# Performance work log

Hardware: AMD Instinct MI355X
Metric: run time of the kernel (lower is better)

Reference implementation:

```python
import jax, jax.numpy as jnp
import numpy as np

N_NODES = 100000
N_EDGES = 1600000
IN_F, HID, EMB = 128, 64, 32


def setup_inputs() -> dict:
    key = jax.random.key(0)
    ks = jax.random.split(key, 10)
    x = jax.random.normal(ks[0], (N_NODES, IN_F), dtype=jnp.float32)
    edge_index = jax.random.randint(ks[1], (2, N_EDGES), 0, N_NODES, dtype=jnp.int64)
    s = lambda k, sh, fan_in: jax.random.normal(k, sh, dtype=jnp.float32) / jnp.sqrt(jnp.float32(fan_in))
    return {
        "x": x,
        "edge_index": edge_index,
        # SAGEConv1: lin_l (applied to aggregated neighbors, with bias) + lin_r (root, no bias)
        "W1_l": s(ks[2], (IN_F, HID), IN_F), "b1": jnp.zeros((HID,), jnp.float32), "W1_r": s(ks[3], (IN_F, HID), IN_F),
        # SAGEConv2
        "W2_l": s(ks[4], (HID, EMB), HID), "b2": jnp.zeros((EMB,), jnp.float32), "W2_r": s(ks[5], (HID, EMB), HID),
        # risk head
        "Wh": s(ks[6], (EMB, 1), EMB), "bh": jnp.zeros((1,), jnp.float32),
    }


def _sage_conv(x, src, dst, W_l, b, W_r):
    # gather messages from source nodes, segment-mean at destination nodes
    msg_sum = jax.ops.segment_sum(x[src], dst, num_segments=N_NODES)  # [N, F]
    cnt = jax.ops.segment_sum(jnp.ones((src.shape[0],), x.dtype), dst, num_segments=N_NODES)
    mean_agg = msg_sum / jnp.maximum(cnt, 1.0)[:, None]  # isolated nodes -> 0
    return mean_agg @ W_l + b + x @ W_r


def reference(x, edge_index, W1_l, b1, W1_r, W2_l, b2, W2_r, Wh, bh):
    src, dst = edge_index[0], edge_index[1]
    h = jax.nn.relu(_sage_conv(x, src, dst, W1_l, b1, W1_r))
    # dropout is identity in eval mode
    embeddings = jax.nn.relu(_sage_conv(h, src, dst, W2_l, b2, W2_r))
    risk_scores = embeddings @ Wh + bh
    return embeddings, risk_scores
```

## Files before the change

kernel.cpp:

```cpp
#include <hip/hip_runtime.h>
#include <hip/hip_bf16.h>

#define N_NODES 100000
#define N_EDGES 1600000
#define NBUCK   196
#define BSHIFT  9
#define BCAP    12288

typedef __bf16 bf16x8 __attribute__((ext_vector_type(8)));
typedef float  f32x4  __attribute__((ext_vector_type(4)));
typedef float  f32x2  __attribute__((ext_vector_type(2)));


__device__ inline unsigned char enc_fp8(float v) {
    return (unsigned char)(__builtin_amdgcn_cvt_pk_fp8_f32(v, v, 0, 0) & 0xFF);
}

__global__ __launch_bounds__(256) void partition_k(const int* __restrict__ ei,
                                                   int* __restrict__ gcur,
                                                   unsigned* __restrict__ bbuf) {
    __shared__ int hist[NBUCK];
    __shared__ int cur[NBUCK];
    int t = threadIdx.x;
    for (int i = t; i < NBUCK; i += 256) hist[i] = 0;
    __syncthreads();
    int base = blockIdx.x * 4096;
    unsigned pk[16];
    int bk[16];
#pragma unroll
    for (int i = 0; i < 16; ++i) {
        int e = base + t + i * 256;
        if (e < N_EDGES) {
            int s = ei[e], d = ei[N_EDGES + e];
            int b = d >> BSHIFT;
            pk[i] = ((unsigned)(d & 511) << 17) | (unsigned)s;
            bk[i] = b;
            atomicAdd(&hist[b], 1);
        } else bk[i] = -1;
    }
    __syncthreads();
    for (int i = t; i < NBUCK; i += 256)
        cur[i] = atomicAdd(&gcur[i], hist[i]);
    __syncthreads();
#pragma unroll
    for (int i = 0; i < 16; ++i) {
        if (bk[i] >= 0) {
            int pos = atomicAdd(&cur[bk[i]], 1);
            bbuf[(size_t)bk[i] * BCAP + pos] = pk[i];
        }
    }
}

__global__ __launch_bounds__(256) void csr_gemm1_k(const unsigned* __restrict__ bbuf,
                                                   const int* __restrict__ gcur,
                                                   int* __restrict__ cnt,
                                                   int* __restrict__ offsets,
                                                   int* __restrict__ csr,
                                                   const float* __restrict__ x,
                                                   const float* __restrict__ W1l,
                                                   const float* __restrict__ W1r,
                                                   unsigned char* __restrict__ c1l,
                                                   __bf16* __restrict__ c1r) {
    __shared__ __align__(16) char smem[34816];
    int t = threadIdx.x;
    if (blockIdx.x < NBUCK) {
        int* lcnt = (int*)smem;
        int* loff = (int*)(smem + 2048);
        int* lcur = (int*)(smem + 4096);
        int* ssum = (int*)(smem + 6144);
        int b = blockIdx.x;
        int m = gcur[b];
        const unsigned* src = bbuf + (size_t)b * BCAP;
        for (int i = t; i < 512; i += 256) lcnt[i] = 0;
        __syncthreads();
        for (int i = t; i < m; i += 256) atomicAdd(&lcnt[src[i] >> 17], 1);
        __syncthreads();
        int a0 = lcnt[2 * t], a1 = lcnt[2 * t + 1];
        int p0 = (a0 + 3) & ~3, p1 = (a1 + 3) & ~3;
        ssum[t] = p0 + p1;
        __syncthreads();
        for (int off = 1; off < 256; off <<= 1) {
            int v = (t >= off) ? ssum[t - off] : 0;
            __syncthreads();
            ssum[t] += v;
            __syncthreads();
        }
        int ebase = (t == 0) ? 0 : ssum[t - 1];
        loff[2 * t] = ebase;
        loff[2 * t + 1] = ebase + p0;
        __syncthreads();
        for (int i = t; i < 512; i += 256) lcur[i] = loff[i];
        int nbase = b << BSHIFT;
        for (int i = t; i < 512; i += 256) {
            int n = nbase + i;
            if (n < N_NODES) {
                cnt[n] = lcnt[i];
                offsets[n] = b * BCAP + loff[i];
            }
        }
        __syncthreads();
        for (int i = t; i < m; i += 256) {
            unsigned p = src[i];
            int pos = atomicAdd(&lcur[p >> 17], 1);
            csr[(size_t)b * BCAP + pos] = (int)(p & 0x1FFFF);
        }
    } else {
        __bf16* Bt = (__bf16*)smem;
        for (int idx = t; idx < 8192; idx += 256) {
            int k = idx >> 6, n = idx & 63;
            Bt[n * 136 + k]        = (__bf16)W1l[idx];
            Bt[(n + 64) * 136 + k] = (__bf16)W1r[idx];
        }
        __syncthreads();

        int lane = t & 63, wave = t >> 6;
        int bid = blockIdx.x - NBUCK;
        int mbase = bid * 64 + wave * 16;
        int col  = lane & 15;
        int kgrp = (lane >> 4) << 3;
        int mrow = mbase + col;
        int mclamp = mrow < N_NODES ? mrow : N_NODES - 1;
        const float* arow = x + (size_t)mclamp * 128;

        f32x4 acc[8];
#pragma unroll
        for (int i = 0; i < 8; ++i) acc[i] = (f32x4){0.f, 0.f, 0.f, 0.f};

#pragma unroll
        for (int ks = 0; ks < 4; ++ks) {
            int kk = ks * 32 + kgrp;
            f32x4 a0 = *(const f32x4*)(arow + kk);
            f32x4 a1 = *(const f32x4*)(arow + kk + 4);
            bf16x8 a;
#pragma unroll
            for (int i = 0; i < 4; ++i) { a[i] = (__bf16)a0[i]; a[i + 4] = (__bf16)a1[i]; }
#pragma unroll
            for (int nt = 0; nt < 8; ++nt) {
                bf16x8 b = *(const bf16x8*)(Bt + (nt * 16 + col) * 136 + kk);
                acc[nt] = __builtin_amdgcn_mfma_f32_16x16x32_bf16(a, b, acc[nt], 0, 0, 0);
            }
        }

        int r0 = mbase + ((lane >> 4) << 2);
#pragma unroll
        for (int r = 0; r < 4; ++r) {
            int m = r0 + r;
            if (m < N_NODES) {
#pragma unroll
                for (int nt = 0; nt < 4; ++nt)
                    c1l[(size_t)m * 64 + nt * 16 + col] = enc_fp8(acc[nt][r]);
#pragma unroll
                for (int nt = 4; nt < 8; ++nt)
                    c1r[(size_t)m * 64 + (nt - 4) * 16 + col] = (__bf16)acc[nt][r];
            }
        }
    }
}

__global__ __launch_bounds__(256) void agg1_gemm2_k(const unsigned char* __restrict__ c1l,
                                                    const __bf16* __restrict__ c1r,
                                                    const int* __restrict__ offsets,
                                                    const int* __restrict__ cnt,
                                                    const int* __restrict__ csr,
                                                    const float* __restrict__ b1,
                                                    const float* __restrict__ W2l,
                                                    const float* __restrict__ W2r,
                                                    unsigned char* __restrict__ c2l,
                                                    float* __restrict__ c2r) {
    __shared__ __bf16 Bt[64 * 72];
    __shared__ __bf16 ht[64 * 72];
    int tid = threadIdx.x;
    for (int idx = tid; idx < 2048; idx += 256) {
        int k = idx >> 5, n = idx & 31;
        Bt[n * 72 + k]        = (__bf16)W2l[idx];
        Bt[(n + 32) * 72 + k] = (__bf16)W2r[idx];
    }

    int lane = tid & 63, wave = tid >> 6;
    int g = lane >> 3;
    int f8b = (lane & 7) << 3;
    f32x4 b1v0 = *(const f32x4*)(b1 + f8b);
    f32x4 b1v1 = *(const f32x4*)(b1 + f8b + 4);
    const int4* csr4 = (const int4*)csr;
#pragma unroll
    for (int p = 0; p < 2; ++p) {
        int lrow = p * 32 + wave * 8 + g;
        int n = blockIdx.x * 64 + lrow;
        bf16x8 o;
        if (n < N_NODES) {
            int beg = offsets[n], deg = cnt[n];
            int end = beg + deg;
            bf16x8 rv = *(const bf16x8*)(c1r + (size_t)n * 64 + f8b);
            float sum[8];
#pragma unroll
            for (int j = 0; j < 8; ++j) sum[j] = 0.f;
            for (int e = beg; e < end; e += 8) {
                int4 i0 = csr4[e >> 2];
                int4 i1 = csr4[(e >> 2) + 1];
                int sidx[8] = {i0.x, i0.y, i0.z, i0.w, i1.x, i1.y, i1.z, i1.w};
                uint2 w[8];
#pragma unroll
                for (int u = 0; u < 8; ++u) {
                    w[u].x = 0u; w[u].y = 0u;
                    if (e + u < end)
                        w[u] = *(const uint2*)(c1l + (size_t)sidx[u] * 64 + f8b);
                }
#pragma unroll
                for (int u = 0; u < 8; ++u) {
                    f32x2 p0 = __builtin_amdgcn_cvt_pk_f32_fp8(w[u].x, 0);
                    f32x2 p1 = __builtin_amdgcn_cvt_pk_f32_fp8(w[u].x, 1);
                    f32x2 p2 = __builtin_amdgcn_cvt_pk_f32_fp8(w[u].y, 0);
                    f32x2 p3 = __builtin_amdgcn_cvt_pk_f32_fp8(w[u].y, 1);
                    sum[0] += p0[0]; sum[1] += p0[1];
                    sum[2] += p1[0]; sum[3] += p1[1];
                    sum[4] += p2[0]; sum[5] += p2[1];
                    sum[6] += p3[0]; sum[7] += p3[1];
                }
            }
            float cf = deg > 0 ? (float)deg : 1.f;
#pragma unroll
            for (int j = 0; j < 8; ++j) {
                float v = sum[j] / cf + (float)rv[j] + ((j < 4) ? b1v0[j] : b1v1[j - 4]);
                o[j] = (__bf16)(v > 0.f ? v : 0.f);
            }
        } else {
#pragma unroll
            for (int j = 0; j < 8; ++j) o[j] = (__bf16)0.f;
        }
        *(bf16x8*)(ht + lrow * 72 + f8b) = o;
    }
    __syncthreads();

    int col  = lane & 15;
    int kgrp = (lane >> 4) << 3;
    int mbase = blockIdx.x * 64 + wave * 16;
    const __bf16* arow = ht + (wave * 16 + col) * 72;

    f32x4 acc[4];
#pragma unroll
    for (int i = 0; i < 4; ++i) acc[i] = (f32x4){0.f, 0.f, 0.f, 0.f};

#pragma unroll
    for (int ks = 0; ks < 2; ++ks) {
        int kk = ks * 32 + kgrp;
        bf16x8 a = *(const bf16x8*)(arow + kk);
#pragma unroll
        for (int nt = 0; nt < 4; ++nt) {
            bf16x8 b = *(const bf16x8*)(Bt + (nt * 16 + col) * 72 + kk);
            acc[nt] = __builtin_amdgcn_mfma_f32_16x16x32_bf16(a, b, acc[nt], 0, 0, 0);
        }
    }

    int r0 = mbase + ((lane >> 4) << 2);
#pragma unroll
    for (int r = 0; r < 4; ++r) {
        int m = r0 + r;
        if (m < N_NODES) {
#pragma unroll
            for (int nt = 0; nt < 2; ++nt)
                c2l[(size_t)m * 32 + nt * 16 + col] = enc_fp8(acc[nt][r]);
#pragma unroll
            for (int nt = 2; nt < 4; ++nt)
                c2r[(size_t)m * 32 + (nt - 2) * 16 + col] = acc[nt][r];
        }
    }
}

__global__ __launch_bounds__(256) void agg2_k(const unsigned char* __restrict__ c2l,
                                              const float* __restrict__ c2r,
                                              const int* __restrict__ offsets,
                                              const int* __restrict__ cnt,
                                              const int* __restrict__ csr,
                                              const float* __restrict__ b2,
                                              const float* __restrict__ Wh,
                                              const float* __restrict__ bh,
                                              float* __restrict__ out) {
    int wave = blockIdx.x * 4 + (threadIdx.x >> 6);
    int lane = threadIdx.x & 63;
    int g = lane >> 2;
    int n = wave * 16 + g;
    int f8b = (lane & 3) << 3;
    bool valid = n < N_NODES;
    int nc = valid ? n : N_NODES - 1;
    int beg = offsets[nc], deg = valid ? cnt[n] : 0;
    int end = beg + deg;
    f32x4 rr0 = *(const f32x4*)(c2r + (size_t)nc * 32 + f8b);
    f32x4 rr1 = *(const f32x4*)(c2r + (size_t)nc * 32 + f8b + 4);
    f32x4 wh0 = *(const f32x4*)(Wh + f8b);
    f32x4 wh1 = *(const f32x4*)(Wh + f8b + 4);
    const int4* csr4 = (const int4*)csr;
    float sum[8];
#pragma unroll
    for (int j = 0; j < 8; ++j) sum[j] = 0.f;
    for (int e = beg; e < end; e += 8) {
        int4 i0 = csr4[e >> 2];
        int4 i1 = csr4[(e >> 2) + 1];
        int sidx[8] = {i0.x, i0.y, i0.z, i0.w, i1.x, i1.y, i1.z, i1.w};
        uint2 w[8];
#pragma unroll
        for (int u = 0; u < 8; ++u) {
            w[u].x = 0u; w[u].y = 0u;
            if (e + u < end)
                w[u] = *(const uint2*)(c2l + (size_t)sidx[u] * 32 + f8b);
        }
#pragma unroll
        for (int u = 0; u < 8; ++u) {
            f32x2 p0 = __builtin_amdgcn_cvt_pk_f32_fp8(w[u].x, 0);
            f32x2 p1 = __builtin_amdgcn_cvt_pk_f32_fp8(w[u].x, 1);
            f32x2 p2 = __builtin_amdgcn_cvt_pk_f32_fp8(w[u].y, 0);
            f32x2 p3 = __builtin_amdgcn_cvt_pk_f32_fp8(w[u].y, 1);
            sum[0] += p0[0]; sum[1] += p0[1];
            sum[2] += p1[0]; sum[3] += p1[1];
            sum[4] += p2[0]; sum[5] += p2[1];
            sum[6] += p3[0]; sum[7] += p3[1];
        }
    }
    float cf = deg > 0 ? (float)deg : 1.f;
    float r = 0.f;
    f32x4 o0, o1;
#pragma unroll
    for (int j = 0; j < 8; ++j) {
        float root = (j < 4) ? rr0[j] : rr1[j - 4];
        float whj  = (j < 4) ? wh0[j] : wh1[j - 4];
        float v = sum[j] / cf + root + b2[f8b + j];
        v = v > 0.f ? v : 0.f;
        if (j < 4) o0[j] = v; else o1[j - 4] = v;
        r += v * whj;
    }
    if (valid) {
        *(f32x4*)(out + (size_t)n * 32 + f8b) = o0;
        *(f32x4*)(out + (size_t)n * 32 + f8b + 4) = o1;
    }
    r += __shfl_xor(r, 1, 64);
    r += __shfl_xor(r, 2, 64);
    if (valid && (lane & 3) == 0)
        out[(size_t)N_NODES * 32 + n] = r + bh[0];
}

extern "C" void kernel_launch(void* const* d_in, const int* in_sizes, int n_in,
                              void* d_out, int out_size, void* d_ws, size_t ws_size,
                              hipStream_t stream) {
    const float* x   = (const float*)d_in[0];
    const int*   ei  = (const int*)d_in[1];
    const float* W1l = (const float*)d_in[2];
    const float* b1  = (const float*)d_in[3];
    const float* W1r = (const float*)d_in[4];
    const float* W2l = (const float*)d_in[5];
    const float* b2  = (const float*)d_in[6];
    const float* W2r = (const float*)d_in[7];
    const float* Wh  = (const float*)d_in[8];
    const float* bh  = (const float*)d_in[9];
    float* out = (float*)d_out;

    char* ws = (char*)d_ws;
    unsigned char* c1l = (unsigned char*)(ws);
    __bf16*   c1r     = (__bf16*)(ws + 6400000);
    unsigned char* c2l = (unsigned char*)(ws + 32000000);
    float*    c2r     = (float*)(ws + 35200000);
    int*      cnt     = (int*)(ws + 48000000);
    int*      offsets = (int*)(ws + 48400000);
    int*      gcur    = (int*)(ws + 48800000);
    unsigned* bbuf    = (unsigned*)(ws + 48804096);
    int*      csr     = (int*)(ws + 58437888);

    hipMemsetAsync(gcur, 0, NBUCK * 4, stream);

    partition_k  <<<391, 256, 0, stream>>>(ei, gcur, bbuf);
    csr_gemm1_k  <<<NBUCK + 1563, 256, 0, stream>>>(bbuf, gcur, cnt, offsets, csr,
                                                    x, W1l, W1r, c1l, c1r);
    agg1_gemm2_k <<<1563, 256, 0, stream>>>(c1l, c1r, offsets, cnt, csr, b1,
                                            W2l, W2r, c2l, c2r);
    agg2_k       <<<1563, 256, 0, stream>>>(c2l, c2r, offsets, cnt, csr, b2, Wh, bh, out);
}
```

Measured before the change: 212.0 us.

## Halve bucket size, prefetch CSR indices, pad shared tile rows

```diff
diff --git a/kernel.cpp b/kernel.cpp
--- a/kernel.cpp
+++ b/kernel.cpp
@@ -3,9 +3,9 @@
 
 #define N_NODES 100000
 #define N_EDGES 1600000
-#define NBUCK   196
-#define BSHIFT  9
-#define BCAP    12288
+#define NBUCK   391
+#define BSHIFT  8
+#define BCAP    6144
 
 typedef __bf16 bf16x8 __attribute__((ext_vector_type(8)));
 typedef float  f32x4  __attribute__((ext_vector_type(4)));
@@ -33,7 +33,7 @@
         if (e < N_EDGES) {
             int s = ei[e], d = ei[N_EDGES + e];
             int b = d >> BSHIFT;
-            pk[i] = ((unsigned)(d & 511) << 17) | (unsigned)s;
+            pk[i] = ((unsigned)(d & 255) << 17) | (unsigned)s;
             bk[i] = b;
             atomicAdd(&hist[b], 1);
         } else bk[i] = -1;
@@ -65,19 +65,17 @@
     int t = threadIdx.x;
     if (blockIdx.x < NBUCK) {
         int* lcnt = (int*)smem;
-        int* loff = (int*)(smem + 2048);
-        int* lcur = (int*)(smem + 4096);
-        int* ssum = (int*)(smem + 6144);
+        int* lcur = (int*)(smem + 1024);
+        int* ssum = (int*)(smem + 2048);
         int b = blockIdx.x;
         int m = gcur[b];
         const unsigned* src = bbuf + (size_t)b * BCAP;
-        for (int i = t; i < 512; i += 256) lcnt[i] = 0;
+        lcnt[t] = 0;
         __syncthreads();
         for (int i = t; i < m; i += 256) atomicAdd(&lcnt[src[i] >> 17], 1);
         __syncthreads();
-        int a0 = lcnt[2 * t], a1 = lcnt[2 * t + 1];
-        int p0 = (a0 + 3) & ~3, p1 = (a1 + 3) & ~3;
-        ssum[t] = p0 + p1;
+        int a0 = lcnt[t];
+        ssum[t] = (a0 + 3) & ~3;
         __syncthreads();
         for (int off = 1; off < 256; off <<= 1) {
             int v = (t >= off) ? ssum[t - off] : 0;
@@ -86,17 +84,11 @@
             __syncthreads();
         }
         int ebase = (t == 0) ? 0 : ssum[t - 1];
-        loff[2 * t] = ebase;
-        loff[2 * t + 1] = ebase + p0;
-        __syncthreads();
-        for (int i = t; i < 512; i += 256) lcur[i] = loff[i];
-        int nbase = b << BSHIFT;
-        for (int i = t; i < 512; i += 256) {
-            int n = nbase + i;
-            if (n < N_NODES) {
-                cnt[n] = lcnt[i];
-                offsets[n] = b * BCAP + loff[i];
-            }
+        lcur[t] = ebase;
+        int n = (b << BSHIFT) + t;
+        if (n < N_NODES) {
+            cnt[n] = a0;
+            offsets[n] = b * BCAP + ebase;
         }
         __syncthreads();
         for (int i = t; i < m; i += 256) {
@@ -168,7 +160,7 @@
                                                     unsigned char* __restrict__ c2l,
                                                     float* __restrict__ c2r) {
     __shared__ __bf16 Bt[64 * 72];
-    __shared__ __bf16 ht[64 * 72];
+    __shared__ __bf16 ht[64 * 76];
     int tid = threadIdx.x;
     for (int idx = tid; idx < 2048; idx += 256) {
         int k = idx >> 5, n = idx & 31;
@@ -191,12 +183,15 @@
             int beg = offsets[n], deg = cnt[n];
             int end = beg + deg;
             bf16x8 rv = *(const bf16x8*)(c1r + (size_t)n * 64 + f8b);
+            int4 j0 = csr4[beg >> 2];
+            int4 j1 = csr4[(beg >> 2) + 1];
             float sum[8];
 #pragma unroll
             for (int j = 0; j < 8; ++j) sum[j] = 0.f;
             for (int e = beg; e < end; e += 8) {
-                int4 i0 = csr4[e >> 2];
-                int4 i1 = csr4[(e >> 2) + 1];
+                int4 i0 = j0, i1 = j1;
+                j0 = csr4[(e >> 2) + 2];
+                j1 = csr4[(e >> 2) + 3];
                 int sidx[8] = {i0.x, i0.y, i0.z, i0.w, i1.x, i1.y, i1.z, i1.w};
                 uint2 w[8];
 #pragma unroll
@@ -227,14 +222,14 @@
 #pragma unroll
             for (int j = 0; j < 8; ++j) o[j] = (__bf16)0.f;
         }
-        *(bf16x8*)(ht + lrow * 72 + f8b) = o;
+        *(bf16x8*)(ht + lrow * 76 + f8b) = o;
     }
     __syncthreads();
 
     int col  = lane & 15;
     int kgrp = (lane >> 4) << 3;
     int mbase = blockIdx.x * 64 + wave * 16;
-    const __bf16* arow = ht + (wave * 16 + col) * 72;
+    const __bf16* arow = ht + (wave * 16 + col) * 76;
 
     f32x4 acc[4];
 #pragma unroll
@@ -289,12 +284,15 @@
     f32x4 wh0 = *(const f32x4*)(Wh + f8b);
     f32x4 wh1 = *(const f32x4*)(Wh + f8b + 4);
     const int4* csr4 = (const int4*)csr;
+    int4 j0 = csr4[beg >> 2];
+    int4 j1 = csr4[(beg >> 2) + 1];
     float sum[8];
 #pragma unroll
     for (int j = 0; j < 8; ++j) sum[j] = 0.f;
     for (int e = beg; e < end; e += 8) {
-        int4 i0 = csr4[e >> 2];
-        int4 i1 = csr4[(e >> 2) + 1];
+        int4 i0 = j0, i1 = j1;
+        j0 = csr4[(e >> 2) + 2];
+        j1 = csr4[(e >> 2) + 3];
         int sidx[8] = {i0.x, i0.y, i0.z, i0.w, i1.x, i1.y, i1.z, i1.w};
         uint2 w[8];
 #pragma unroll
```

Result: faster. 204.5 us (median of 2 runs) (-3.6%).
